# Performance work log

Hardware: AMD Instinct MI355X
Metric: run time of the kernel (lower is better)

The kernel has to match this reference:

```python
import jax, jax.numpy as jnp
import numpy as np

NUM_USERS = 100000
NUM_ITEMS = 50000
EMBED_DIM = 64
N_LAYERS = 3
N_EDGES = 4000000
BATCH = 1024
N_NODES = NUM_USERS + NUM_ITEMS


def setup_inputs() -> dict:
    key = jax.random.key(0)
    k1, k2, k3, k4, k5, k6 = jax.random.split(key, 6)
    user_emb = jax.random.normal(k1, (NUM_USERS, EMBED_DIM), dtype=jnp.float32) * 0.1
    item_emb = jax.random.normal(k2, (NUM_ITEMS, EMBED_DIM), dtype=jnp.float32) * 0.1
    # COO representation of the symmetric-normalized adjacency (values ~ 1/sqrt(di*dj))
    edge_val = jax.random.uniform(k3, (N_EDGES,), dtype=jnp.float32)
    edge_src = jax.random.randint(k4, (N_EDGES,), 0, N_NODES, dtype=jnp.int32)
    edge_dst = jax.random.randint(k5, (N_EDGES,), 0, N_NODES, dtype=jnp.int32)
    users = jax.random.randint(k6, (BATCH,), 0, NUM_USERS, dtype=jnp.int32)
    return {
        "user_emb": user_emb,
        "item_emb": item_emb,
        "edge_val": edge_val,
        "edge_src": edge_src,
        "edge_dst": edge_dst,
        "users": users,
    }


def reference(user_emb, item_emb, edge_val, edge_src, edge_dst, users):
    # computer(): layer-wise sparse propagation with running sum (mean at the end)
    all_emb = jnp.concatenate([user_emb, item_emb], axis=0)  # [N, D]
    acc = all_emb
    emb = all_emb
    for _ in range(N_LAYERS):
        # SpMM: out[i] = sum_{(i,j) in E} val_ij * emb[j]
        msg = emb[edge_dst] * edge_val[:, None]               # [E, D] gather
        emb = jax.ops.segment_sum(msg, edge_src, num_segments=N_NODES)
        acc = acc + emb
    light_out = acc / jnp.float32(N_LAYERS + 1)               # mean over stacked layers
    all_users = light_out[:NUM_USERS]
    all_items = light_out[NUM_USERS:]
    # get_user_ratings(): batch of users scored against all items
    user_embeds = all_users[users]                            # [B, D]
    ratings = user_embeds @ all_items.T                       # [B, num_items]
    return ratings
```

## Files before the change

kernel.cpp:

```cpp
#include <hip/hip_runtime.h>
#include <hip/hip_fp16.h>

#define NUM_USERS 100000
#define NUM_ITEMS 50000
#define EMBED_DIM 64
#define N_NODES 150000
#define N_EDGES 4000000
#define N_LAYERS 3
#define BATCH 1024

#define NBKT 293
#define CHUNK 8192
#define NBLK_A ((N_EDGES + CHUNK - 1) / CHUNK)

typedef float f32x4 __attribute__((ext_vector_type(4)));
typedef _Float16 f16x8 __attribute__((ext_vector_type(8)));
typedef float f32x4a __attribute__((ext_vector_type(4)));

__global__ void clear_uflag_kernel(int* __restrict__ uflag) {
    int i = blockIdx.x * blockDim.x + threadIdx.x;
    if (i < NUM_USERS) uflag[i] = 0;
}

__global__ void mark_users_kernel(const int* __restrict__ users, int* __restrict__ uflag) {
    int i = blockIdx.x * blockDim.x + threadIdx.x;
    if (i < BATCH) uflag[users[i]] = 1;
}

__global__ void init_emb_kernel(const float* __restrict__ ue, const float* __restrict__ ie,
                                const int* __restrict__ uflag,
                                float* __restrict__ acc, __half2* __restrict__ h0) {
    int i = blockIdx.x * blockDim.x + threadIdx.x;
    const int total  = N_NODES * (EMBED_DIM / 4);
    const int usplit = NUM_USERS * (EMBED_DIM / 4);
    if (i < total) {
        float4 v = (i < usplit) ? reinterpret_cast<const float4*>(ue)[i]
                                : reinterpret_cast<const float4*>(ie)[i - usplit];
        h0[i * 2 + 0] = __float22half2_rn(make_float2(v.x, v.y));
        h0[i * 2 + 1] = __float22half2_rn(make_float2(v.z, v.w));
        int n = i >> 4;
        if (n >= NUM_USERS || uflag[n])
            reinterpret_cast<float4*>(acc)[i] = v;
    }
}

__global__ void histA_kernel(const int* __restrict__ src, int* __restrict__ hist) {
    __shared__ int lcnt[NBKT];
    int blk = blockIdx.x, t = threadIdx.x;
    for (int b = t; b < NBKT; b += 256) lcnt[b] = 0;
    __syncthreads();
    int e0 = blk * CHUNK;
    for (int i = t; i < CHUNK; i += 256) {
        int e = e0 + i;
        if (e < N_EDGES) atomicAdd(&lcnt[src[e] >> 9], 1);
    }
    __syncthreads();
    for (int b = t; b < NBKT; b += 256) hist[blk * NBKT + b] = lcnt[b];
}

__global__ void scanA_kernel(const int* __restrict__ hist, int* __restrict__ off,
                             int* __restrict__ bucketTotal) {
    __shared__ int s[512];
    int b = blockIdx.x, t = threadIdx.x;
    int v0 = (t < NBLK_A) ? hist[t * NBKT + b] : 0;
    s[t] = v0;
    __syncthreads();
    for (int o = 1; o < 512; o <<= 1) {
        int v = (t >= o) ? s[t - o] : 0;
        __syncthreads();
        s[t] += v;
        __syncthreads();
    }
    if (t < NBLK_A) off[t * NBKT + b] = s[t] - v0;
    if (t == NBLK_A - 1) bucketTotal[b] = s[t];
}

__global__ void scanB_kernel(const int* __restrict__ bucketTotal, int* __restrict__ bucketBase,
                             int* __restrict__ rowptr) {
    __shared__ int s[512];
    int t = threadIdx.x;
    s[t] = (t < NBKT) ? bucketTotal[t] : 0;
    __syncthreads();
    for (int o = 1; o < 512; o <<= 1) {
        int v = (t >= o) ? s[t - o] : 0;
        __syncthreads();
        s[t] += v;
        __syncthreads();
    }
    if (t < NBKT) bucketBase[t] = (t > 0) ? s[t - 1] : 0;
    if (t == 0) { bucketBase[NBKT] = s[NBKT - 1]; rowptr[N_NODES] = N_EDGES; }
}

__global__ void partA3_kernel(const int* __restrict__ src, const int* __restrict__ dst,
                              const float* __restrict__ val, const int* __restrict__ off,
                              const int* __restrict__ bucketBase, int2* __restrict__ tmp) {
    __shared__ int lcnt[NBKT];
    int blk = blockIdx.x, t = threadIdx.x;
    for (int b = t; b < NBKT; b += 256) lcnt[b] = 0;
    __syncthreads();
    int e0 = blk * CHUNK;
    for (int i = t; i < CHUNK; i += 256) {
        int e = e0 + i;
        if (e < N_EDGES) {
            int s = src[e];
            int b = s >> 9;
            int r = atomicAdd(&lcnt[b], 1);
            int pos = bucketBase[b] + off[blk * NBKT + b] + r;
            tmp[pos] = make_int2(dst[e] | ((s & 511) << 18), __float_as_int(val[e]));
        }
    }
}

__global__ void passB_kernel(const int2* __restrict__ tmp, const int* __restrict__ bucketBase,
                             int* __restrict__ rowptr, int2* __restrict__ edge_s) {
    __shared__ int sdeg[512];
    __shared__ int cursor[512];
    int bkt = blockIdx.x;
    int t = threadIdx.x;
    int base = bucketBase[bkt];
    int cntE = bucketBase[bkt + 1] - base;
    sdeg[t] = 0;
    __syncthreads();
    for (int i = t; i < cntE; i += 512)
        atomicAdd(&sdeg[tmp[base + i].x >> 18], 1);
    __syncthreads();
    int d = sdeg[t];
    for (int o = 1; o < 512; o <<= 1) {
        int v = (t >= o) ? sdeg[t - o] : 0;
        __syncthreads();
        sdeg[t] += v;
        __syncthreads();
    }
    int excl = sdeg[t] - d;
    cursor[t] = excl;
    int n = (bkt << 9) + t;
    if (n < N_NODES) rowptr[n] = base + excl;
    __syncthreads();
    for (int i = t; i < cntE; i += 512) {
        int2 e = tmp[base + i];
        int p = base + atomicAdd(&cursor[e.x >> 18], 1);
        edge_s[p] = make_int2(e.x & 0x3FFFF, e.y);
    }
}

template <bool WRITE_NXT>
__global__ void gather_layer_kernel(const __half* __restrict__ emb, const int* __restrict__ rowptr,
                                    const int2* __restrict__ eg, const int* __restrict__ uflag,
                                    __half* __restrict__ nxt, float* __restrict__ acc) {
    int tid = blockIdx.x * 256 + threadIdx.x;
    int n = tid >> 3;
    if (n >= N_NODES) return;
    bool needed = (n >= NUM_USERS) || uflag[n];
    if (!WRITE_NXT && !needed) return;
    int c = (tid & 7) * 8;
    int beg = rowptr[n];
    int end = rowptr[n + 1];
    float a0 = 0.f, a1 = 0.f, a2 = 0.f, a3 = 0.f;
    float a4 = 0.f, a5 = 0.f, a6 = 0.f, a7 = 0.f;
    int j = beg;
    for (; j + 4 <= end; j += 4) {
        int2 e0 = eg[j];     int2 e1 = eg[j + 1];
        int2 e2 = eg[j + 2]; int2 e3 = eg[j + 3];
        uint4 r0 = *reinterpret_cast<const uint4*>(emb + (long)e0.x * EMBED_DIM + c);
        uint4 r1 = *reinterpret_cast<const uint4*>(emb + (long)e1.x * EMBED_DIM + c);
        uint4 r2 = *reinterpret_cast<const uint4*>(emb + (long)e2.x * EMBED_DIM + c);
        uint4 r3 = *reinterpret_cast<const uint4*>(emb + (long)e3.x * EMBED_DIM + c);
        float v0 = __int_as_float(e0.y), v1 = __int_as_float(e1.y);
        float v2 = __int_as_float(e2.y), v3 = __int_as_float(e3.y);
#define ACC8(R, V)                                                              \
        {                                                                       \
            const __half2* hp = reinterpret_cast<const __half2*>(&R);           \
            float2 f0 = __half22float2(hp[0]); float2 f1 = __half22float2(hp[1]);\
            float2 f2 = __half22float2(hp[2]); float2 f3 = __half22float2(hp[3]);\
            a0 += f0.x * V; a1 += f0.y * V; a2 += f1.x * V; a3 += f1.y * V;     \
            a4 += f2.x * V; a5 += f2.y * V; a6 += f3.x * V; a7 += f3.y * V;     \
        }
        ACC8(r0, v0) ACC8(r1, v1) ACC8(r2, v2) ACC8(r3, v3)
    }
    for (; j < end; ++j) {
        int2 e0 = eg[j];
        uint4 r0 = *reinterpret_cast<const uint4*>(emb + (long)e0.x * EMBED_DIM + c);
        float v0 = __int_as_float(e0.y);
        ACC8(r0, v0)
    }
#undef ACC8
    if (WRITE_NXT) {
        uint4 o;
        __half2* op = reinterpret_cast<__half2*>(&o);
        op[0] = __float22half2_rn(make_float2(a0, a1));
        op[1] = __float22half2_rn(make_float2(a2, a3));
        op[2] = __float22half2_rn(make_float2(a4, a5));
        op[3] = __float22half2_rn(make_float2(a6, a7));
        *reinterpret_cast<uint4*>(nxt + (long)n * EMBED_DIM + c) = o;
    }
    if (needed) {
        float* ap = acc + (long)n * EMBED_DIM + c;
        float4 x0 = *reinterpret_cast<float4*>(ap);
        float4 x1 = *reinterpret_cast<float4*>(ap + 4);
        x0.x += a0; x0.y += a1; x0.z += a2; x0.w += a3;
        x1.x += a4; x1.y += a5; x1.z += a6; x1.w += a7;
        *reinterpret_cast<float4*>(ap)     = x0;
        *reinterpret_cast<float4*>(ap + 4) = x1;
    }
}

__global__ void pack_ab_kernel(const float* __restrict__ acc, const int* __restrict__ users,
                               __half* __restrict__ A16, __half* __restrict__ B16) {
    int tid = blockIdx.x * 256 + threadIdx.x;
    const int total = (BATCH + NUM_ITEMS) * 8;
    if (tid >= total) return;
    int r = tid >> 3;
    int c = (tid & 7) * 8;
    const float* src;
    __half* dstp;
    if (r < BATCH) {
        src  = acc + (long)users[r] * EMBED_DIM + c;
        dstp = A16 + (long)r * EMBED_DIM + c;
    } else {
        int i = r - BATCH;
        src  = acc + (long)(NUM_USERS + i) * EMBED_DIM + c;
        dstp = B16 + (long)i * EMBED_DIM + c;
    }
    float4 v0 = *reinterpret_cast<const float4*>(src);
    float4 v1 = *reinterpret_cast<const float4*>(src + 4);
    uint4 o;
    __half2* op = reinterpret_cast<__half2*>(&o);
    op[0] = __float22half2_rn(make_float2(v0.x, v0.y));
    op[1] = __float22half2_rn(make_float2(v0.z, v0.w));
    op[2] = __float22half2_rn(make_float2(v1.x, v1.y));
    op[3] = __float22half2_rn(make_float2(v1.z, v1.w));
    *reinterpret_cast<uint4*>(dstp) = o;
}

__global__ __launch_bounds__(256)
void ratings_mfma_kernel(const __half* __restrict__ A16, const __half* __restrict__ B16,
                         float* __restrict__ out) {
    const int w  = threadIdx.x >> 6;
    const int l  = threadIdx.x & 63;
    const int u0 = blockIdx.y * 32 + (w & 1) * 16;
    const int i0 = blockIdx.x * 128 + (w >> 1) * 64;
    const int row = l & 15;
    const int kq  = (l >> 4) * 8;

    f32x4a acc0 = {0.f, 0.f, 0.f, 0.f};
    f32x4a acc1 = {0.f, 0.f, 0.f, 0.f};
    f32x4a acc2 = {0.f, 0.f, 0.f, 0.f};
    f32x4a acc3 = {0.f, 0.f, 0.f, 0.f};

#pragma unroll
    for (int ks = 0; ks < EMBED_DIM; ks += 32) {
        f16x8 a = *reinterpret_cast<const f16x8*>(A16 + (long)(u0 + row) * EMBED_DIM + ks + kq);
        int ir0 = i0 + 0 * 16 + row; if (ir0 >= NUM_ITEMS) ir0 = NUM_ITEMS - 1;
        int ir1 = i0 + 1 * 16 + row; if (ir1 >= NUM_ITEMS) ir1 = NUM_ITEMS - 1;
        int ir2 = i0 + 2 * 16 + row; if (ir2 >= NUM_ITEMS) ir2 = NUM_ITEMS - 1;
        int ir3 = i0 + 3 * 16 + row; if (ir3 >= NUM_ITEMS) ir3 = NUM_ITEMS - 1;
        f16x8 b0 = *reinterpret_cast<const f16x8*>(B16 + (long)ir0 * EMBED_DIM + ks + kq);
        f16x8 b1 = *reinterpret_cast<const f16x8*>(B16 + (long)ir1 * EMBED_DIM + ks + kq);
        f16x8 b2 = *reinterpret_cast<const f16x8*>(B16 + (long)ir2 * EMBED_DIM + ks + kq);
        f16x8 b3 = *reinterpret_cast<const f16x8*>(B16 + (long)ir3 * EMBED_DIM + ks + kq);
        acc0 = __builtin_amdgcn_mfma_f32_16x16x32_f16(a, b0, acc0, 0, 0, 0);
        acc1 = __builtin_amdgcn_mfma_f32_16x16x32_f16(a, b1, acc1, 0, 0, 0);
        acc2 = __builtin_amdgcn_mfma_f32_16x16x32_f16(a, b2, acc2, 0, 0, 0);
        acc3 = __builtin_amdgcn_mfma_f32_16x16x32_f16(a, b3, acc3, 0, 0, 0);
    }

    const float inv = 1.0f / 16.0f;
    const int orow = u0 + (l >> 4) * 4;
    const int colb = l & 15;
#define STORE_FRAG(ACC, C)                                                      \
    {                                                                           \
        int col = i0 + (C) * 16 + colb;                                         \
        if (col < NUM_ITEMS) {                                                  \
            __builtin_nontemporal_store(ACC[0] * inv, out + (long)(orow + 0) * NUM_ITEMS + col); \
            __builtin_nontemporal_store(ACC[1] * inv, out + (long)(orow + 1) * NUM_ITEMS + col); \
            __builtin_nontemporal_store(ACC[2] * inv, out + (long)(orow + 2) * NUM_ITEMS + col); \
            __builtin_nontemporal_store(ACC[3] * inv, out + (long)(orow + 3) * NUM_ITEMS + col); \
        }                                                                       \
    }
    STORE_FRAG(acc0, 0)
    STORE_FRAG(acc1, 1)
    STORE_FRAG(acc2, 2)
    STORE_FRAG(acc3, 3)
#undef STORE_FRAG
}

extern "C" void kernel_launch(void* const* d_in, const int* in_sizes, int n_in,
                              void* d_out, int out_size, void* d_ws, size_t ws_size,
                              hipStream_t stream) {
    const float* ue    = (const float*)d_in[0];
    const float* ie    = (const float*)d_in[1];
    const float* val   = (const float*)d_in[2];
    const int*   src   = (const int*)d_in[3];
    const int*   dst   = (const int*)d_in[4];
    const int*   users = (const int*)d_in[5];
    float* out = (float*)d_out;

    const size_t tab = (size_t)N_NODES * EMBED_DIM;
    float*  acc   = (float*)d_ws;
    __half* h0    = (__half*)(acc + tab);
    __half* h1    = h0 + tab;
    int*    uflag = (int*)(h1 + tab);

    __half* A16 = h1;
    __half* B16 = h1 + (size_t)BATCH * EMBED_DIM;

    char* ob = (char*)d_out;
    int2* edge_s      = (int2*)(ob);
    int2* tmp         = (int2*)(ob + (64u << 20));
    int*  hist        = (int*) (ob + (96u << 20));
    int*  off         = (int*) (ob + (98u << 20));
    int*  bucketTotal = (int*) (ob + (100u << 20));
    int*  bucketBase  = (int*) (ob + (101u << 20));
    int*  rowptr      = (int*) (ob + (102u << 20));

    clear_uflag_kernel<<<(NUM_USERS + 255) / 256, 256, 0, stream>>>(uflag);
    mark_users_kernel<<<(BATCH + 255) / 256, 256, 0, stream>>>(users, uflag);

    const int totalv = N_NODES * EMBED_DIM / 4;
    init_emb_kernel<<<(totalv + 255) / 256, 256, 0, stream>>>(ue, ie, uflag, acc, (__half2*)h0);

    histA_kernel <<<NBLK_A, 256, 0, stream>>>(src, hist);
    scanA_kernel <<<NBKT, 512, 0, stream>>>(hist, off, bucketTotal);
    scanB_kernel <<<1, 512, 0, stream>>>(bucketTotal, bucketBase, rowptr);
    partA3_kernel<<<NBLK_A, 256, 0, stream>>>(src, dst, val, off, bucketBase, tmp);
    passB_kernel <<<NBKT, 512, 0, stream>>>(tmp, bucketBase, rowptr, edge_s);

    const int ggrid = (N_NODES * 8 + 255) / 256;
    gather_layer_kernel<true><<<ggrid, 256, 0, stream>>>(h0, rowptr, edge_s, uflag, h1, acc);
    gather_layer_kernel<true><<<ggrid, 256, 0, stream>>>(h1, rowptr, edge_s, uflag, h0, acc);
    gather_layer_kernel<false><<<ggrid, 256, 0, stream>>>(h0, rowptr, edge_s, uflag, h1, acc);

    const int packn = (BATCH + NUM_ITEMS) * 8;
    pack_ab_kernel<<<(packn + 255) / 256, 256, 0, stream>>>(acc, users, A16, B16);

    dim3 rgrid((NUM_ITEMS + 127) / 128, BATCH / 32);
    ratings_mfma_kernel<<<rgrid, 256, 0, stream>>>(A16, B16, out);
}
```

Before: 389.4 us.

## Quantize edge weights, sort edges by destination slice, slice-synchronized persistent gather

Edge records are packed into a single 32-bit word holding an 18-bit destination and a 14-bit quantized weight, which halves edge-stream traffic. Edges within each row are sorted by destination slice. The gather kernel now runs as a fixed grid of 1024 blocks, each thread handling 5 nodes, and steps through destination slices with a block barrier after each slice so the embedding rows being gathered stay in cache. The last layer writes fp16 output directly, and the ratings kernel indexes users and items from that table, which removes the pack kernel. The weight quantization adds approximation error, and the per-slice barriers can serialize the work.

Result: slower. 737.5 us (+89.4%).

```diff
diff --git a/kernel.cpp b/kernel.cpp
--- a/kernel.cpp
+++ b/kernel.cpp
@@ -12,6 +12,13 @@
 #define NBKT 293
 #define CHUNK 8192
 #define NBLK_A ((N_EDGES + CHUNK - 1) / CHUNK)
+
+#define NSLICE 10
+#define NKEY (512 * 16)
+
+#define GBLK 1024
+#define NGRP (GBLK * 32)
+#define NPT 5
 
 typedef float f32x4 __attribute__((ext_vector_type(4)));
 typedef _Float16 f16x8 __attribute__((ext_vector_type(8)));
@@ -106,134 +113,143 @@
             int b = s >> 9;
             int r = atomicAdd(&lcnt[b], 1);
             int pos = bucketBase[b] + off[blk * NBKT + b] + r;
-            tmp[pos] = make_int2(dst[e] | ((s & 511) << 18), __float_as_int(val[e]));
+            int q = (int)(val[e] * 16384.0f);
+            if (q > 16383) q = 16383;
+            tmp[pos] = make_int2(s & 511, dst[e] | (q << 18));
         }
     }
 }
 
-__global__ void passB_kernel(const int2* __restrict__ tmp, const int* __restrict__ bucketBase,
-                             int* __restrict__ rowptr, int2* __restrict__ edge_s) {
-    __shared__ int sdeg[512];
-    __shared__ int cursor[512];
+__global__ __launch_bounds__(512)
+void passB_kernel(const int2* __restrict__ tmp, const int* __restrict__ bucketBase,
+                  int* __restrict__ rowptr, unsigned* __restrict__ edge_s) {
+    __shared__ int sdeg[NKEY];
+    __shared__ int cur[NKEY];
+    __shared__ int ttot[512];
     int bkt = blockIdx.x;
     int t = threadIdx.x;
     int base = bucketBase[bkt];
     int cntE = bucketBase[bkt + 1] - base;
-    sdeg[t] = 0;
-    __syncthreads();
-    for (int i = t; i < cntE; i += 512)
-        atomicAdd(&sdeg[tmp[base + i].x >> 18], 1);
-    __syncthreads();
-    int d = sdeg[t];
-    for (int o = 1; o < 512; o <<= 1) {
-        int v = (t >= o) ? sdeg[t - o] : 0;
-        __syncthreads();
-        sdeg[t] += v;
-        __syncthreads();
-    }
-    int excl = sdeg[t] - d;
-    cursor[t] = excl;
-    int n = (bkt << 9) + t;
-    if (n < N_NODES) rowptr[n] = base + excl;
+    for (int k = t; k < NKEY; k += 512) sdeg[k] = 0;
     __syncthreads();
     for (int i = t; i < cntE; i += 512) {
         int2 e = tmp[base + i];
-        int p = base + atomicAdd(&cursor[e.x >> 18], 1);
-        edge_s[p] = make_int2(e.x & 0x3FFFF, e.y);
+        int key = (e.x << 4) | ((e.y & 0x3FFFF) >> 14);
+        atomicAdd(&sdeg[key], 1);
+    }
+    __syncthreads();
+    int run = 0;
+    int k0 = t * 16;
+#pragma unroll
+    for (int i = 0; i < 16; ++i) { int v = sdeg[k0 + i]; sdeg[k0 + i] = run; run += v; }
+    ttot[t] = run;
+    __syncthreads();
+    for (int o = 1; o < 512; o <<= 1) {
+        int v = (t >= o) ? ttot[t - o] : 0;
+        __syncthreads();
+        ttot[t] += v;
+        __syncthreads();
+    }
+    int texcl = ttot[t] - run;
+#pragma unroll
+    for (int i = 0; i < 16; ++i) { int v = sdeg[k0 + i] + texcl; sdeg[k0 + i] = v; cur[k0 + i] = v; }
+    int n = (bkt << 9) + t;
+    if (n < N_NODES) rowptr[n] = base + texcl;
+    __syncthreads();
+    for (int i = t; i < cntE; i += 512) {
+        int2 e = tmp[base + i];
+        int key = (e.x << 4) | ((e.y & 0x3FFFF) >> 14);
+        int p = base + atomicAdd(&cur[key], 1);
+        edge_s[p] = (unsigned)e.y;
     }
 }
 
 template <bool WRITE_NXT>
-__global__ void gather_layer_kernel(const __half* __restrict__ emb, const int* __restrict__ rowptr,
-                                    const int2* __restrict__ eg, const int* __restrict__ uflag,
-                                    __half* __restrict__ nxt, float* __restrict__ acc) {
-    int tid = blockIdx.x * 256 + threadIdx.x;
-    int n = tid >> 3;
-    if (n >= N_NODES) return;
-    bool needed = (n >= NUM_USERS) || uflag[n];
-    if (!WRITE_NXT && !needed) return;
-    int c = (tid & 7) * 8;
-    int beg = rowptr[n];
-    int end = rowptr[n + 1];
-    float a0 = 0.f, a1 = 0.f, a2 = 0.f, a3 = 0.f;
-    float a4 = 0.f, a5 = 0.f, a6 = 0.f, a7 = 0.f;
-    int j = beg;
-    for (; j + 4 <= end; j += 4) {
-        int2 e0 = eg[j];     int2 e1 = eg[j + 1];
-        int2 e2 = eg[j + 2]; int2 e3 = eg[j + 3];
-        uint4 r0 = *reinterpret_cast<const uint4*>(emb + (long)e0.x * EMBED_DIM + c);
-        uint4 r1 = *reinterpret_cast<const uint4*>(emb + (long)e1.x * EMBED_DIM + c);
-        uint4 r2 = *reinterpret_cast<const uint4*>(emb + (long)e2.x * EMBED_DIM + c);
-        uint4 r3 = *reinterpret_cast<const uint4*>(emb + (long)e3.x * EMBED_DIM + c);
-        float v0 = __int_as_float(e0.y), v1 = __int_as_float(e1.y);
-        float v2 = __int_as_float(e2.y), v3 = __int_as_float(e3.y);
-#define ACC8(R, V)                                                              \
-        {                                                                       \
-            const __half2* hp = reinterpret_cast<const __half2*>(&R);           \
-            float2 f0 = __half22float2(hp[0]); float2 f1 = __half22float2(hp[1]);\
-            float2 f2 = __half22float2(hp[2]); float2 f3 = __half22float2(hp[3]);\
-            a0 += f0.x * V; a1 += f0.y * V; a2 += f1.x * V; a3 += f1.y * V;     \
-            a4 += f2.x * V; a5 += f2.y * V; a6 += f3.x * V; a7 += f3.y * V;     \
+__global__ __launch_bounds__(256, 4)
+void gather_layer_kernel(const __half* __restrict__ emb, const int* __restrict__ rowptr,
+                         const unsigned* __restrict__ eg, const int* __restrict__ uflag,
+                         __half* __restrict__ outp, float* __restrict__ acc) {
+    const int t = threadIdx.x;
+    const int g = blockIdx.x * 32 + (t >> 3);
+    const int c = (t & 7) * 8;
+
+    float a[NPT][8];
+    int jc[NPT], je[NPT];
+    bool nd[NPT];
+#pragma unroll
+    for (int q = 0; q < NPT; ++q) {
+        int n = q * NGRP + g;
+        bool ok = n < N_NODES;
+        bool need = ok && ((n >= NUM_USERS) || uflag[n]);
+        nd[q] = need;
+        int beg = 0, end = 0;
+        if (ok && (WRITE_NXT || need)) { beg = rowptr[n]; end = rowptr[n + 1]; }
+        jc[q] = beg; je[q] = end;
+#pragma unroll
+        for (int i = 0; i < 8; ++i) a[q][i] = 0.f;
+    }
+
+    for (int sl = 0; sl < NSLICE; ++sl) {
+        int hi = (sl + 1) << 14;
+#pragma unroll
+        for (int q = 0; q < NPT; ++q) {
+            int j = jc[q], e2 = je[q];
+            while (j < e2) {
+                unsigned ew = eg[j];
+                int d = ew & 0x3FFFF;
+                if (d >= hi) break;
+                float v = ((float)(ew >> 18) + 0.5f) * 6.103515625e-5f;
+                uint4 r = *reinterpret_cast<const uint4*>(emb + (long)d * EMBED_DIM + c);
+                const __half2* hp = reinterpret_cast<const __half2*>(&r);
+                float2 f0 = __half22float2(hp[0]); float2 f1 = __half22float2(hp[1]);
+                float2 f2 = __half22float2(hp[2]); float2 f3 = __half22float2(hp[3]);
+                a[q][0] += f0.x * v; a[q][1] += f0.y * v; a[q][2] += f1.x * v; a[q][3] += f1.y * v;
+                a[q][4] += f2.x * v; a[q][5] += f2.y * v; a[q][6] += f3.x * v; a[q][7] += f3.y * v;
+                ++j;
+            }
+            jc[q] = j;
         }
-        ACC8(r0, v0) ACC8(r1, v1) ACC8(r2, v2) ACC8(r3, v3)
-    }
-    for (; j < end; ++j) {
-        int2 e0 = eg[j];
-        uint4 r0 = *reinterpret_cast<const uint4*>(emb + (long)e0.x * EMBED_DIM + c);
-        float v0 = __int_as_float(e0.y);
-        ACC8(r0, v0)
-    }
-#undef ACC8
-    if (WRITE_NXT) {
-        uint4 o;
-        __half2* op = reinterpret_cast<__half2*>(&o);
-        op[0] = __float22half2_rn(make_float2(a0, a1));
-        op[1] = __float22half2_rn(make_float2(a2, a3));
-        op[2] = __float22half2_rn(make_float2(a4, a5));
-        op[3] = __float22half2_rn(make_float2(a6, a7));
-        *reinterpret_cast<uint4*>(nxt + (long)n * EMBED_DIM + c) = o;
-    }
-    if (needed) {
-        float* ap = acc + (long)n * EMBED_DIM + c;
-        float4 x0 = *reinterpret_cast<float4*>(ap);
-        float4 x1 = *reinterpret_cast<float4*>(ap + 4);
-        x0.x += a0; x0.y += a1; x0.z += a2; x0.w += a3;
-        x1.x += a4; x1.y += a5; x1.z += a6; x1.w += a7;
-        *reinterpret_cast<float4*>(ap)     = x0;
-        *reinterpret_cast<float4*>(ap + 4) = x1;
-    }
-}
-
-__global__ void pack_ab_kernel(const float* __restrict__ acc, const int* __restrict__ users,
-                               __half* __restrict__ A16, __half* __restrict__ B16) {
-    int tid = blockIdx.x * 256 + threadIdx.x;
-    const int total = (BATCH + NUM_ITEMS) * 8;
-    if (tid >= total) return;
-    int r = tid >> 3;
-    int c = (tid & 7) * 8;
-    const float* src;
-    __half* dstp;
-    if (r < BATCH) {
-        src  = acc + (long)users[r] * EMBED_DIM + c;
-        dstp = A16 + (long)r * EMBED_DIM + c;
-    } else {
-        int i = r - BATCH;
-        src  = acc + (long)(NUM_USERS + i) * EMBED_DIM + c;
-        dstp = B16 + (long)i * EMBED_DIM + c;
-    }
-    float4 v0 = *reinterpret_cast<const float4*>(src);
-    float4 v1 = *reinterpret_cast<const float4*>(src + 4);
-    uint4 o;
-    __half2* op = reinterpret_cast<__half2*>(&o);
-    op[0] = __float22half2_rn(make_float2(v0.x, v0.y));
-    op[1] = __float22half2_rn(make_float2(v0.z, v0.w));
-    op[2] = __float22half2_rn(make_float2(v1.x, v1.y));
-    op[3] = __float22half2_rn(make_float2(v1.z, v1.w));
-    *reinterpret_cast<uint4*>(dstp) = o;
+        __syncthreads();
+    }
+
+#pragma unroll
+    for (int q = 0; q < NPT; ++q) {
+        int n = q * NGRP + g;
+        if (n >= N_NODES) continue;
+        if (WRITE_NXT) {
+            uint4 o;
+            __half2* op = reinterpret_cast<__half2*>(&o);
+            op[0] = __float22half2_rn(make_float2(a[q][0], a[q][1]));
+            op[1] = __float22half2_rn(make_float2(a[q][2], a[q][3]));
+            op[2] = __float22half2_rn(make_float2(a[q][4], a[q][5]));
+            op[3] = __float22half2_rn(make_float2(a[q][6], a[q][7]));
+            *reinterpret_cast<uint4*>(outp + (long)n * EMBED_DIM + c) = o;
+            if (nd[q]) {
+                float* ap = acc + (long)n * EMBED_DIM + c;
+                float4 x0 = *reinterpret_cast<float4*>(ap);
+                float4 x1 = *reinterpret_cast<float4*>(ap + 4);
+                x0.x += a[q][0]; x0.y += a[q][1]; x0.z += a[q][2]; x0.w += a[q][3];
+                x1.x += a[q][4]; x1.y += a[q][5]; x1.z += a[q][6]; x1.w += a[q][7];
+                *reinterpret_cast<float4*>(ap)     = x0;
+                *reinterpret_cast<float4*>(ap + 4) = x1;
+            }
+        } else if (nd[q]) {
+            const float* ap = acc + (long)n * EMBED_DIM + c;
+            float4 x0 = *reinterpret_cast<const float4*>(ap);
+            float4 x1 = *reinterpret_cast<const float4*>(ap + 4);
+            uint4 o;
+            __half2* op = reinterpret_cast<__half2*>(&o);
+            op[0] = __float22half2_rn(make_float2(x0.x + a[q][0], x0.y + a[q][1]));
+            op[1] = __float22half2_rn(make_float2(x0.z + a[q][2], x0.w + a[q][3]));
+            op[2] = __float22half2_rn(make_float2(x1.x + a[q][4], x1.y + a[q][5]));
+            op[3] = __float22half2_rn(make_float2(x1.z + a[q][6], x1.w + a[q][7]));
+            *reinterpret_cast<uint4*>(outp + (long)n * EMBED_DIM + c) = o;
+        }
+    }
 }
 
 __global__ __launch_bounds__(256)
-void ratings_mfma_kernel(const __half* __restrict__ A16, const __half* __restrict__ B16,
+void ratings_mfma_kernel(const __half* __restrict__ T16, const int* __restrict__ users,
                          float* __restrict__ out) {
     const int w  = threadIdx.x >> 6;
     const int l  = threadIdx.x & 63;
@@ -241,23 +257,25 @@
     const int i0 = blockIdx.x * 128 + (w >> 1) * 64;
     const int row = l & 15;
     const int kq  = (l >> 4) * 8;
+    const int uid = users[u0 + row];
 
     f32x4a acc0 = {0.f, 0.f, 0.f, 0.f};
     f32x4a acc1 = {0.f, 0.f, 0.f, 0.f};
     f32x4a acc2 = {0.f, 0.f, 0.f, 0.f};
     f32x4a acc3 = {0.f, 0.f, 0.f, 0.f};
 
+    int ir0 = i0 + 0 * 16 + row; if (ir0 >= NUM_ITEMS) ir0 = NUM_ITEMS - 1;
+    int ir1 = i0 + 1 * 16 + row; if (ir1 >= NUM_ITEMS) ir1 = NUM_ITEMS - 1;
+    int ir2 = i0 + 2 * 16 + row; if (ir2 >= NUM_ITEMS) ir2 = NUM_ITEMS - 1;
+    int ir3 = i0 + 3 * 16 + row; if (ir3 >= NUM_ITEMS) ir3 = NUM_ITEMS - 1;
+
 #pragma unroll
     for (int ks = 0; ks < EMBED_DIM; ks += 32) {
-        f16x8 a = *reinterpret_cast<const f16x8*>(A16 + (long)(u0 + row) * EMBED_DIM + ks + kq);
-        int ir0 = i0 + 0 * 16 + row; if (ir0 >= NUM_ITEMS) ir0 = NUM_ITEMS - 1;
-        int ir1 = i0 + 1 * 16 + row; if (ir1 >= NUM_ITEMS) ir1 = NUM_ITEMS - 1;
-        int ir2 = i0 + 2 * 16 + row; if (ir2 >= NUM_ITEMS) ir2 = NUM_ITEMS - 1;
-        int ir3 = i0 + 3 * 16 + row; if (ir3 >= NUM_ITEMS) ir3 = NUM_ITEMS - 1;
-        f16x8 b0 = *reinterpret_cast<const f16x8*>(B16 + (long)ir0 * EMBED_DIM + ks + kq);
-        f16x8 b1 = *reinterpret_cast<const f16x8*>(B16 + (long)ir1 * EMBED_DIM + ks + kq);
-        f16x8 b2 = *reinterpret_cast<const f16x8*>(B16 + (long)ir2 * EMBED_DIM + ks + kq);
-        f16x8 b3 = *reinterpret_cast<const f16x8*>(B16 + (long)ir3 * EMBED_DIM + ks + kq);
+        f16x8 a = *reinterpret_cast<const f16x8*>(T16 + (long)uid * EMBED_DIM + ks + kq);
+        f16x8 b0 = *reinterpret_cast<const f16x8*>(T16 + (long)(NUM_USERS + ir0) * EMBED_DIM + ks + kq);
+        f16x8 b1 = *reinterpret_cast<const f16x8*>(T16 + (long)(NUM_USERS + ir1) * EMBED_DIM + ks + kq);
+        f16x8 b2 = *reinterpret_cast<const f16x8*>(T16 + (long)(NUM_USERS + ir2) * EMBED_DIM + ks + kq);
+        f16x8 b3 = *reinterpret_cast<const f16x8*>(T16 + (long)(NUM_USERS + ir3) * EMBED_DIM + ks + kq);
         acc0 = __builtin_amdgcn_mfma_f32_16x16x32_f16(a, b0, acc0, 0, 0, 0);
         acc1 = __builtin_amdgcn_mfma_f32_16x16x32_f16(a, b1, acc1, 0, 0, 0);
         acc2 = __builtin_amdgcn_mfma_f32_16x16x32_f16(a, b2, acc2, 0, 0, 0);
@@ -301,11 +319,8 @@
     __half* h1    = h0 + tab;
     int*    uflag = (int*)(h1 + tab);
 
-    __half* A16 = h1;
-    __half* B16 = h1 + (size_t)BATCH * EMBED_DIM;
-
     char* ob = (char*)d_out;
-    int2* edge_s      = (int2*)(ob);
+    unsigned* edge_s  = (unsigned*)(ob);
     int2* tmp         = (int2*)(ob + (64u << 20));
     int*  hist        = (int*) (ob + (96u << 20));
     int*  off         = (int*) (ob + (98u << 20));
@@ -325,14 +340,10 @@
     partA3_kernel<<<NBLK_A, 256, 0, stream>>>(src, dst, val, off, bucketBase, tmp);
     passB_kernel <<<NBKT, 512, 0, stream>>>(tmp, bucketBase, rowptr, edge_s);
 
-    const int ggrid = (N_NODES * 8 + 255) / 256;
-    gather_layer_kernel<true><<<ggrid, 256, 0, stream>>>(h0, rowptr, edge_s, uflag, h1, acc);
-    gather_layer_kernel<true><<<ggrid, 256, 0, stream>>>(h1, rowptr, edge_s, uflag, h0, acc);
-    gather_layer_kernel<false><<<ggrid, 256, 0, stream>>>(h0, rowptr, edge_s, uflag, h1, acc);
-
-    const int packn = (BATCH + NUM_ITEMS) * 8;
-    pack_ab_kernel<<<(packn + 255) / 256, 256, 0, stream>>>(acc, users, A16, B16);
+    gather_layer_kernel<true ><<<GBLK, 256, 0, stream>>>(h0, rowptr, edge_s, uflag, h1, acc);
+    gather_layer_kernel<true ><<<GBLK, 256, 0, stream>>>(h1, rowptr, edge_s, uflag, h0, acc);
+    gather_layer_kernel<false><<<GBLK, 256, 0, stream>>>(h0, rowptr, edge_s, uflag, h1, acc);
 
     dim3 rgrid((NUM_ITEMS + 127) / 128, BATCH / 32);
-    ratings_mfma_kernel<<<rgrid, 256, 0, stream>>>(A16, B16, out);
-}
+    ratings_mfma_kernel<<<rgrid, 256, 0, stream>>>(h1, users, out);
+}
```
